# Kernel optimization log

Hardware: AMD Instinct MI355X
Metric: run time of the kernel (lower is better)

Reference implementation:

```python
import jax, jax.numpy as jnp
import numpy as np

ZONEOUT = 0.1  # eval-mode zoneout: deterministic mix prob*h_prev + (1-prob)*h_new
R = 2          # reduction_factor


def _lstm_zoneout(x, h, c, wih, whh, bih, bhh):
    g = x @ wih.T + bih + h @ whh.T + bhh
    i, f, gg, o = jnp.split(g, 4, axis=-1)
    c2 = jax.nn.sigmoid(f) * c + jax.nn.sigmoid(i) * jnp.tanh(gg)
    h2 = jax.nn.sigmoid(o) * jnp.tanh(c2)
    return ZONEOUT * h + (1 - ZONEOUT) * h2, ZONEOUT * c + (1 - ZONEOUT) * c2


def setup_inputs() -> dict:
    key = jax.random.key(0)
    ks = jax.random.split(key, 20)
    B, TENC, ENC, DEC = 64, 200, 256, 1024
    HATT, CONV, K = 128, 32, 31
    PRE, C, TFEAT = 256, 80, 1000
    s = 0.05
    def w(k, shape):
        return jax.random.normal(k, shape, jnp.float32) * s
    inp = {}
    inp['enc_output'] = jax.random.normal(ks[0], (B, TENC, ENC), jnp.float32)
    inp['text_len'] = jax.random.randint(ks[1], (B,), TENC // 2, TENC + 1, jnp.int32)
    inp['feature_target'] = jax.random.normal(ks[2], (B, C, TFEAT), jnp.float32)
    inp['att_fc_enc_w'] = w(ks[3], (HATT, ENC)); inp['att_fc_enc_b'] = jnp.zeros((HATT,), jnp.float32)
    inp['att_fc_dec_w'] = w(ks[4], (HATT, DEC))
    inp['att_fc_att_w'] = w(ks[5], (HATT, CONV))
    inp['att_loc_conv_w'] = w(ks[6], (CONV, 1, K))
    inp['att_w_w'] = w(ks[7], (1, HATT)); inp['att_w_b'] = jnp.zeros((1,), jnp.float32)
    inp['prenet_w0'] = w(ks[8], (PRE, C * R)); inp['prenet_b0'] = jnp.zeros((PRE,), jnp.float32)
    inp['prenet_w1'] = w(ks[9], (PRE, PRE)); inp['prenet_b1'] = jnp.zeros((PRE,), jnp.float32)
    inp['lstm0_wih'] = w(ks[10], (4 * DEC, ENC + PRE)); inp['lstm0_whh'] = w(ks[11], (4 * DEC, DEC))
    inp['lstm0_bih'] = jnp.zeros((4 * DEC,), jnp.float32); inp['lstm0_bhh'] = jnp.zeros((4 * DEC,), jnp.float32)
    inp['lstm1_wih'] = w(ks[12], (4 * DEC, DEC)); inp['lstm1_whh'] = w(ks[13], (4 * DEC, DEC))
    inp['lstm1_bih'] = jnp.zeros((4 * DEC,), jnp.float32); inp['lstm1_bhh'] = jnp.zeros((4 * DEC,), jnp.float32)
    inp['feat_out_w'] = w(ks[14], (C * R, ENC + DEC))
    inp['prob_out_w'] = w(ks[15], (R, ENC + DEC)); inp['prob_out_b'] = jnp.zeros((R,), jnp.float32)
    return inp


def reference(enc_output, text_len, feature_target,
              att_fc_enc_w, att_fc_enc_b, att_fc_dec_w, att_fc_att_w, att_loc_conv_w, att_w_w, att_w_b,
              prenet_w0, prenet_b0, prenet_w1, prenet_b1,
              lstm0_wih, lstm0_whh, lstm0_bih, lstm0_bhh,
              lstm1_wih, lstm1_whh, lstm1_bih, lstm1_bhh,
              feat_out_w, prob_out_w, prob_out_b):
    B, TENC, ENC = enc_output.shape
    C, T = feature_target.shape[1], feature_target.shape[2]
    S = T // R  # decoder steps (teacher forcing)
    ft = feature_target.transpose(0, 2, 1).reshape(B, S, C * R)
    pad = (att_loc_conv_w.shape[-1] - 1) // 2
    pm = enc_output @ att_fc_enc_w.T + att_fc_enc_b  # processed memory (B,T,H)
    mask = jnp.arange(TENC)[None, :] >= text_len[:, None]  # pad mask (B,T)
    DEC = lstm0_whh.shape[1]

    def attend(h0, att_prev):
        conv = jax.lax.conv_general_dilated(att_prev[:, None, :], att_loc_conv_w, (1,), [(pad, pad)],
                                            dimension_numbers=('NCH', 'OIH', 'NCH'))  # (B,conv,T)
        conv = jnp.einsum('bct,hc->bth', conv, att_fc_att_w)
        e = jnp.tanh(conv + pm + (h0 @ att_fc_dec_w.T)[:, None, :]) @ att_w_w.T + att_w_b  # (B,T,1)
        e = jnp.where(mask, -jnp.inf, e[..., 0])
        aw = jax.nn.softmax(e, axis=1)
        ac = jnp.einsum('bt,btc->bc', aw, enc_output)
        return ac, aw

    def one_step(h0, c0, h1, c1, att_prev, prev_out):
        ac, aw = attend(h0, att_prev)
        p = jax.nn.relu(prev_out @ prenet_w0.T + prenet_b0)
        p = jax.nn.relu(p @ prenet_w1.T + prenet_b1)
        xs = jnp.concatenate([ac, p], axis=1)
        h0, c0 = _lstm_zoneout(xs, h0, c0, lstm0_wih, lstm0_whh, lstm0_bih, lstm0_bhh)
        h1, c1 = _lstm_zoneout(h0, h1, c1, lstm1_wih, lstm1_whh, lstm1_bih, lstm1_bhh)
        hcs = jnp.concatenate([h1, ac], axis=1)
        return h0, c0, h1, c1, aw, hcs @ feat_out_w.T, hcs @ prob_out_w.T + prob_out_b

    z = jnp.zeros((B, DEC), enc_output.dtype)
    go = jnp.zeros((B, C * R), enc_output.dtype)
    tl = text_len[:, None].astype(enc_output.dtype)
    uniform = (~mask).astype(enc_output.dtype) / tl  # initial prev_att_w

    # step 0: uniform attention prior, go-frame input; afterwards acc = att_w (not uniform+att_w)
    h0, c0, h1, c1, aw0, out0, log0 = one_step(z, z, z, z, uniform, go)

    def scan_step(carry, prev_out):
        h0, c0, h1, c1, acc = carry
        h0, c0, h1, c1, aw, out, logit = one_step(h0, c0, h1, c1, acc, prev_out)
        return (h0, c0, h1, c1, acc + aw), (out, logit, aw)

    _, (outs, logits, aws) = jax.lax.scan(scan_step, (h0, c0, h1, c1, aw0), ft[:, :S - 1, :].transpose(1, 0, 2))
    outs = jnp.concatenate([out0[None], outs], axis=0)    # (S,B,C*R)
    logits = jnp.concatenate([log0[None], logits], axis=0)  # (S,B,R)
    aws = jnp.concatenate([aw0[None], aws], axis=0)       # (S,B,T)
    output = outs.transpose(1, 0, 2).reshape(B, S * R, C).transpose(0, 2, 1)  # (B,C,S*R)
    logit = logits.transpose(1, 0, 2).reshape(B, S * R)
    att_w = aws.transpose(1, 0, 2)  # (B,S,T)
    return output, logit, att_w
```

## Files before the change

kernel.cpp:

```cpp
#include <hip/hip_runtime.h>

#define SS 500
#define NBLKS 256
#define NSLOT 64
#define DYN_LDS 141824
#define RING 32

typedef __bf16 bf16_t;
typedef bf16_t bf16x8 __attribute__((ext_vector_type(8)));
typedef float floatx4 __attribute__((ext_vector_type(4)));

union ABu { uint4 u4; bf16x8 v; unsigned short us[8]; };

#define MFMA(a,b,c) __builtin_amdgcn_mfma_f32_16x16x32_bf16((a),(b),(c),0,0,0)

__device__ __forceinline__ float b2f(unsigned short u){
  union { unsigned int ui; float f; } x; x.ui = ((unsigned int)u) << 16; return x.f;
}
__device__ __forceinline__ unsigned short f2b(float f){
  union { float f; unsigned int ui; } x; x.f = f;
  unsigned int r = x.ui + 0x7FFFu + ((x.ui >> 16) & 1u);
  return (unsigned short)(r >> 16);
}
__device__ __forceinline__ float sigf(float x){ return 1.f/(1.f + __expf(-x)); }
__device__ __forceinline__ float tanhf_fast(float x){
  x = fminf(fmaxf(x, -15.f), 15.f);
  float e = __expf(2.f*x);
  return (e - 1.f)/(e + 1.f);
}

__device__ __forceinline__ void st_sc(unsigned short* p, unsigned short v){
  unsigned int w32 = v;
  asm volatile("global_store_short %0, %1, off sc0 sc1" :: "v"(p), "v"(w32) : "memory");
}

__device__ __forceinline__ void gbar(unsigned int* slots, unsigned int* flag,
                                     unsigned int ep, int is_master){
  asm volatile("s_waitcnt vmcnt(0)" ::: "memory");
  __syncthreads();
  if (threadIdx.x == 0){
    __hip_atomic_fetch_add(&slots[(blockIdx.x & (NSLOT-1)) * 32], 1u,
                           __ATOMIC_RELAXED, __HIP_MEMORY_SCOPE_AGENT);
  }
  if (is_master){
    if (threadIdx.x < 64){
      for(;;){
        unsigned int v = __hip_atomic_load(&slots[threadIdx.x * 32],
                                           __ATOMIC_RELAXED, __HIP_MEMORY_SCOPE_AGENT);
        int t = (int)v;
        t += __shfl_xor(t, 1);  t += __shfl_xor(t, 2);  t += __shfl_xor(t, 4);
        t += __shfl_xor(t, 8);  t += __shfl_xor(t, 16); t += __shfl_xor(t, 32);
        if ((unsigned int)t >= ep * NBLKS) break;
        __builtin_amdgcn_s_sleep(1);
      }
      __hip_atomic_store(&flag[threadIdx.x * 32], ep,
                         __ATOMIC_RELAXED, __HIP_MEMORY_SCOPE_AGENT);
    }
  } else {
    if (threadIdx.x == 0){
      unsigned int* myf = &flag[(blockIdx.x & (NSLOT-1)) * 32];
      while (__hip_atomic_load(myf, __ATOMIC_RELAXED, __HIP_MEMORY_SCOPE_AGENT) < ep)
        __builtin_amdgcn_s_sleep(2);
    }
  }
  __syncthreads();
  asm volatile("" ::: "memory");
}


__global__ void k_pm(const float* __restrict__ enc, const float* __restrict__ ew,
                     const float* __restrict__ eb, unsigned short* __restrict__ pmT){
  int id = blockIdx.x*256 + threadIdx.x;
  if (id >= 64*200*128) return;
  int h = id & 127; int bt = id >> 7;
  const float* er = enc + (size_t)bt*256;
  const float* wr = ew + (size_t)h*256;
  float a0=eb[h], a1=0.f, a2=0.f, a3=0.f;
  for (int k=0;k<256;k+=4){
    a0 += er[k]*wr[k]; a1 += er[k+1]*wr[k+1]; a2 += er[k+2]*wr[k+2]; a3 += er[k+3]*wr[k+3];
  }
  int b = bt / 200, t = bt - b*200;
  pmT[(size_t)b*25600 + (size_t)h*200 + t] = f2b((a0+a1)+(a2+a3));
}

__global__ void k_encT(const float* __restrict__ enc, unsigned short* __restrict__ encT){
  int id = blockIdx.x*256 + threadIdx.x;
  if (id >= 64*256*200) return;
  int t = id % 200; int c = (id / 200) & 255; int b = id / 51200;
  encT[id] = f2b(enc[((size_t)b*200 + t)*256 + c]);
}

__global__ void k_w2f(const float* __restrict__ attw, const float* __restrict__ convw,
                      unsigned short* __restrict__ w2f){
  __shared__ float s_w2[128*31];
  int tid = threadIdx.x;
  for (int i = tid; i < 128*31; i += 256){
    int h = i / 31, k = i % 31;
    float v = 0.f;
    for (int c=0;c<32;++c) v += attw[h*32+c]*convw[c*31+k];
    s_w2[i] = v;
  }
  __syncthreads();
  for (int i = tid; i < 512; i += 256){
    int nt = i >> 6, lane = i & 63;
    int h = nt*16 + (lane&15);
    for (int j=0;j<8;++j){
      int k = (lane>>4)*8 + j;
      w2f[(nt*64+lane)*8+j] = f2b(k < 31 ? s_w2[h*31+k] : 0.f);
    }
  }
}

__global__ void k_packlstm(const float* __restrict__ wih, const float* __restrict__ whh,
                           unsigned short* __restrict__ dst, int Kih, int NKS){
  int id = blockIdx.x*256 + threadIdx.x;
  if (id >= 128*NKS*64) return;
  int lane = id & 63; int t = id >> 6; int cu = t / NKS;
  for (int nt=0; nt<2; ++nt){
    int n = nt*16 + (lane&15);
    int du = n>>2, g = n&3;
    int row = g*1024 + cu*8 + du;
    for (int j=0;j<8;++j){
      int k = (t % NKS)*32 + ((lane>>4)*8) + j;
      float v = (k < Kih) ? wih[(size_t)row*Kih + k] : whh[(size_t)row*1024 + (k - Kih)];
      dst[((size_t)(t*2+nt)*64 + lane)*8 + j] = f2b(v);
    }
  }
}

__global__ void k_bias(const float* bi0,const float* bh0,const float* bi1,const float* bh1,
                       float* b0p, float* b1p){
  int id = blockIdx.x*256 + threadIdx.x;
  if (id >= 4096) return;
  int cu = id>>5, n = id&31, du = n>>2, g = n&3;
  int row = g*1024 + cu*8 + du;
  b0p[id] = bi0[row] + bh0[row];
  b1p[id] = bi1[row] + bh1[row];
}

__global__ void k_packgen(const float* __restrict__ src, unsigned short* __restrict__ dst,
                          int N, int K){
  int tot = (N/16)*(K/32)*64;
  int id = blockIdx.x*256 + threadIdx.x;
  if (id >= tot) return;
  int lane = id & 63; int t = id >> 6;
  int nks = K/32;
  int n = (t / nks)*16 + (lane&15);
  for (int j=0;j<8;++j){
    int k = (t % nks)*32 + (lane>>4)*8 + j;
    dst[((size_t)t*64 + lane)*8 + j] = f2b(src[(size_t)n*K + k]);
  }
}

__global__ void k_woutp(const float* __restrict__ fw, const float* __restrict__ pw,
                        unsigned short* __restrict__ dst){
  int id = blockIdx.x*256 + threadIdx.x;
  if (id >= 11*40*64) return;
  int lane = id & 63; int t = id >> 6;
  int n = (t/40)*16 + (lane&15);
  for (int j=0;j<8;++j){
    int k = (t%40)*32 + (lane>>4)*8 + j;
    float v = 0.f;
    if (n < 160) v = fw[(size_t)n*1280 + k];
    else if (n < 162) v = pw[(size_t)(n-160)*1280 + k];
    dst[((size_t)t*64 + lane)*8 + j] = f2b(v);
  }
}

__global__ void k_pre1(const float* __restrict__ ftgt, const unsigned short* __restrict__ w0p,
                       const float* __restrict__ b0, unsigned short* __restrict__ C1){
  int mt = blockIdx.x;
  int tid = threadIdx.x, w = tid>>6, L = tid&63, ccol = L&15, q = L>>4;
  int sb0 = mt*16; int s = sb0 >> 6; int b0r = sb0 & 63;
  floatx4 z = {0.f,0.f,0.f,0.f};
  floatx4 acc[4] = {z,z,z,z};
  for (int ks=0; ks<5; ++ks){
    ABu av;
    if (s == 0){ av.u4.x=0; av.u4.y=0; av.u4.z=0; av.u4.w=0; }
    else {
      int b = b0r + ccol;
      for (int j=0;j<8;++j){
        int jj = ks*32 + q*8 + j;
        av.us[j] = f2b(ftgt[(size_t)b*80000 + (size_t)(jj%80)*1000 + (size_t)(s-1)*2 + (jj/80)]);
      }
    }
    for (int i=0;i<4;++i){
      ABu bf; bf.u4 = *(const uint4*)(w0p + ((size_t)((w*4+i)*5 + ks)*64 + L)*8);
      acc[i] = MFMA(av.v, bf.v, acc[i]);
    }
  }
  for (int i=0;i<4;++i){
    int icol = (w*4+i)*16 + ccol;
    float bia = b0[icol];
    for (int r=0;r<4;++r){
      int sb = sb0 + q*4 + r;
      C1[(size_t)sb*256 + icol] = f2b(fmaxf(acc[i][r] + bia, 0.f));
    }
  }
}

__global__ void k_pre2(const unsigned short* __restrict__ C1, const unsigned short* __restrict__ w1p,
                       const float* __restrict__ b1, unsigned short* __restrict__ P){
  int mt = blockIdx.x;
  int tid = threadIdx.x, w = tid>>6, L = tid&63, ccol = L&15, q = L>>4;
  int sb0 = mt*16;
  floatx4 z = {0.f,0.f,0.f,0.f};
  floatx4 acc[4] = {z,z,z,z};
  for (int ks=0; ks<8; ++ks){
    ABu av; av.u4 = *(const uint4*)(C1 + (size_t)(sb0+ccol)*256 + ks*32 + q*8);
    for (int i=0;i<4;++i){
      ABu bf; bf.u4 = *(const uint4*)(w1p + ((size_t)((w*4+i)*8 + ks)*64 + L)*8);
      acc[i] = MFMA(av.v, bf.v, acc[i]);
    }
  }
  for (int i=0;i<4;++i){
    int icol = (w*4+i)*16 + ccol;
    float bia = b1[icol];
    for (int r=0;r<4;++r){
      int sb = sb0 + q*4 + r;
      P[(size_t)sb*256 + icol] = f2b(fmaxf(acc[i][r] + bia, 0.f));
    }
  }
}


struct PArgs {
  const int* tlen;
  const float* ww; const float* wwb; const float* probb;
  const unsigned short* pmT; const unsigned short* encT;
  const unsigned short* W2f; const unsigned short* Wdecf;
  const unsigned short* W0p; const unsigned short* W1p;
  const float* b0p; const float* b1p;
  const unsigned short* P; const unsigned short* Woutp;
  unsigned short* xh0; unsigned short* xh1; unsigned short* acbf;
  unsigned int* bar; unsigned int* flag;
  float* dout;
};

__global__ __launch_bounds__(256, 1) void k_decoder(PArgs A)
{
  const int cu = blockIdx.x;
  const int tid = threadIdx.x;
  const int w = tid>>6, L = tid&63;
  const int ccol = L&15, q = L>>4;
  const int is_master = (cu == NBLKS-1);

  extern __shared__ char pool[];
  unsigned short* sW = (unsigned short*)pool;
  float* sGB; float* sCST; float* sBIAS;
  if (cu < 128){
    sGB   = (float*)(pool + 98304);
    sCST  = (float*)(pool + 106752);
    sBIAS = (float*)(pool + 108800);
  } else {
    sGB   = (float*)(pool + 131072);
    sCST  = (float*)(pool + 139520);
    sBIAS = (float*)(pool + 141568);
  }

  __shared__ unsigned short s_ahi[240], s_alo[240];
  __shared__ unsigned short s_h0[1024];
  __shared__ float s_e[256];
  __shared__ float s_red[16];
  __shared__ float s_dp[128];
  __shared__ float s_ww[128];

  if (cu < 128){
    const unsigned short* src = A.W0p + (size_t)cu*48*2*512;
    for (int i = tid*8; i < 48*2*512; i += 2048)
      *(uint4*)(sW + i) = *(const uint4*)(src + i);
    if (tid < 32) sBIAS[tid] = A.b0p[cu*32 + tid];
  } else {
    const unsigned short* src = A.W1p + (size_t)(cu-128)*64*2*512;
    for (int i = tid*8; i < 64*2*512; i += 2048)
      *(uint4*)(sW + i) = *(const uint4*)(src + i);
    if (tid < 32) sBIAS[tid] = A.b1p[(cu-128)*32 + tid];
  }
  for (int i = tid; i < 512; i += 256) sCST[i] = 0.f;

  float accv = 0.f; int lenb = 0; float wwbv = 0.f;
  ABu w2fr[8];
  if (cu < 64) {
    lenb = A.tlen[cu];
    wwbv = A.wwb[0];
    float inv = 1.f / (float)lenb;
    for (int i = tid; i < 240; i += 256) {
      int t = i - 15;
      float v = (t >= 0 && t < 200 && t < lenb) ? inv : 0.f;
      unsigned short hi = f2b(v);
      s_ahi[i] = hi; s_alo[i] = f2b(v - b2f(hi));
    }
    if (tid < 200) accv = (tid < lenb) ? inv : 0.f;
    if (tid < 128) s_ww[tid] = A.ww[tid];
    #pragma unroll
    for (int nt=0; nt<8; ++nt) w2fr[nt].u4 = *(const uint4*)(A.W2f + (nt*64 + L)*8);
  }

  unsigned int ep = 0;
  gbar(A.bar, A.flag, ++ep, is_master);
  __builtin_amdgcn_fence(__ATOMIC_ACQUIRE, "agent");

  for (int s = 0; s <= SS+1; ++s) {
    if (cu < 64 && s < SS) {
      const int b = cu;
      const unsigned short* xh0r = A.xh0 + (size_t)((s+RING-1)&(RING-1))*65536;
      if (tid < 128) *(uint4*)(s_h0 + tid*8) = *(const uint4*)(xh0r + b*1024 + tid*8);
      __syncthreads();
      {
        uint4 p0[8], p1[8];
        #pragma unroll
        for (int k=0;k<8;++k){
          p0[k] = *(const uint4*)(A.Wdecf + (size_t)((w*2+0)*32+k)*512 + (size_t)L*8);
          p1[k] = *(const uint4*)(A.Wdecf + (size_t)((w*2+1)*32+k)*512 + (size_t)L*8);
        }
        floatx4 acc0 = {0.f,0.f,0.f,0.f}, acc1 = {0.f,0.f,0.f,0.f};
        #pragma unroll
        for (int ks=0; ks<32; ++ks){
          ABu bf0, bf1; bf0.u4 = p0[ks&7]; bf1.u4 = p1[ks&7];
          if (ks+8 < 32){
            p0[ks&7] = *(const uint4*)(A.Wdecf + (size_t)((w*2+0)*32+ks+8)*512 + (size_t)L*8);
            p1[ks&7] = *(const uint4*)(A.Wdecf + (size_t)((w*2+1)*32+ks+8)*512 + (size_t)L*8);
          }
          ABu av;
          if (ccol == 0) av.u4 = *(const uint4*)(s_h0 + ks*32 + q*8);
          else { av.u4.x=0; av.u4.y=0; av.u4.z=0; av.u4.w=0; }
          acc0 = MFMA(av.v, bf0.v, acc0);
          acc1 = MFMA(av.v, bf1.v, acc1);
        }
        if (L < 16){
          s_dp[(w*2+0)*16 + ccol] = acc0[0];
          s_dp[(w*2+1)*16 + ccol] = acc1[0];
        }
      }
      __syncthreads();
      {
        const unsigned short* pmrowT = A.pmT + (size_t)b*25600;
        for (int mt = w; mt < 13; mt += 4) {
          ABu ahi, alo;
          int abase = mt*16 + ccol + q*8;
          for (int j=0;j<8;++j){ ahi.us[j] = s_ahi[abase+j]; alo.us[j] = s_alo[abase+j]; }
          floatx4 acc[8];
          for (int nt=0;nt<8;++nt){
            floatx4 zz = {0.f,0.f,0.f,0.f};
            zz = MFMA(ahi.v, w2fr[nt].v, zz);
            zz = MFMA(alo.v, w2fr[nt].v, zz);
            acc[nt] = zz;
          }
          int t0 = mt*16 + q*4;
          union { ushort4 v; unsigned short us[4]; } pv[8];
          #pragma unroll
          for (int nt=0;nt<8;++nt)
            pv[nt].v = *(const ushort4*)(pmrowT + (size_t)(nt*16+ccol)*200 + t0);
          #pragma unroll
          for (int r=0;r<4;++r){
            int t = t0 + r;
            float part = 0.f;
            if (t < 200) {
              #pragma unroll
              for (int nt=0;nt<8;++nt){
                int h = nt*16 + ccol;
                float v = acc[nt][r] + b2f(pv[nt].us[r]) + s_dp[h];
                part += s_ww[h] * tanhf_fast(v);
              }
            }
            part += __shfl_xor(part, 1);
            part += __shfl_xor(part, 2);
            part += __shfl_xor(part, 4);
            part += __shfl_xor(part, 8);
            if (t < 200 && ccol == 0)
              s_e[t] = (t < lenb) ? (part + wwbv) : -1e30f;
          }
        }
      }
      __syncthreads();
      {
        float v = (tid < 200) ? s_e[tid] : -1e30f;
        float m = v;
        for (int o=1;o<64;o<<=1) m = fmaxf(m, __shfl_xor(m, o));
        if (L == 0) s_red[w] = m;
        __syncthreads();
        m = fmaxf(fmaxf(s_red[0], s_red[1]), fmaxf(s_red[2], s_red[3]));
        float ex = (tid < 200) ? __expf(v - m) : 0.f;
        float sm = ex;
        for (int o=1;o<64;o<<=1) sm += __shfl_xor(sm, o);
        if (L == 0) s_red[8+w] = sm;
        __syncthreads();
        float inv = 1.f / (s_red[8]+s_red[9]+s_red[10]+s_red[11]);
        if (tid < 200){
          float aw = ex * inv;
          s_e[tid] = aw;
          A.dout[5184000 + (size_t)b*100000 + (size_t)s*200 + tid] = aw;
          accv = (s == 0) ? aw : (accv + aw);
          unsigned short hi = f2b(accv);
          s_ahi[15+tid] = hi; s_alo[15+tid] = f2b(accv - b2f(hi));
        }
      }
      __syncthreads();
      {
        const unsigned short* er = A.encT + (size_t)b*51200 + (size_t)tid*200;
        float a0=0.f,a1=0.f,a2=0.f,a3=0.f;
        #pragma unroll 5
        for (int it=0; it<25; ++it){
          ABu v; v.u4 = *(const uint4*)(er + it*8);
          a0 += s_e[it*8+0]*b2f(v.us[0]); a1 += s_e[it*8+1]*b2f(v.us[1]);
          a2 += s_e[it*8+2]*b2f(v.us[2]); a3 += s_e[it*8+3]*b2f(v.us[3]);
          a0 += s_e[it*8+4]*b2f(v.us[4]); a1 += s_e[it*8+5]*b2f(v.us[5]);
          a2 += s_e[it*8+6]*b2f(v.us[6]); a3 += s_e[it*8+7]*b2f(v.us[7]);
        }
        st_sc(A.acbf + (size_t)(s&(RING-1))*16384 + b*256 + tid, f2b((a0+a1)+(a2+a3)));
      }
    }
    if (cu >= 75 && cu < 119 && s >= 2) {
      const int nt = (cu-75) % 11; const int mg = (cu-75) / 11;
      const int s2 = s - 2;
      const unsigned short* segH  = A.xh1 + (size_t)(s2&(RING-1))*65536;
      const unsigned short* segAC = A.acbf + (size_t)(s2&(RING-1))*16384;
      const unsigned short* wo = A.Woutp + (size_t)nt*40*512;
      const int brow = mg*16 + ccol;
      uint4 ap[10], wp[10];
      #pragma unroll
      for (int kk=0; kk<10; ++kk){
        int ks = w*10 + kk;
        ap[kk] = *(const uint4*)((ks < 32) ? (segH + (size_t)brow*1024 + ks*32 + q*8)
                                           : (segAC + (size_t)brow*256 + (ks-32)*32 + q*8));
        wp[kk] = *(const uint4*)(wo + (size_t)ks*512 + (size_t)L*8);
      }
      floatx4 acc = {0.f,0.f,0.f,0.f};
      #pragma unroll
      for (int kk=0; kk<10; ++kk){
        ABu av, bf; av.u4 = ap[kk]; bf.u4 = wp[kk];
        acc = MFMA(av.v, bf.v, acc);
      }
      #pragma unroll
      for (int r=0;r<4;++r) sGB[w*256 + (q*4+r)*16 + ccol] = acc[r];
      __syncthreads();
      {
        float v = sGB[tid] + sGB[256+tid] + sGB[512+tid] + sGB[768+tid];
        int blocal = tid>>4, colp = tid&15;
        int j = nt*16 + colp; int bb = mg*16 + blocal;
        if (j < 160){
          int rr = j/80, cc2 = j%80;
          A.dout[(size_t)bb*80000 + (size_t)cc2*1000 + s2*2 + rr] = v;
        } else if (j < 162){
          A.dout[5120000 + (size_t)bb*1000 + s2*2 + (j-160)] = v + A.probb[j-160];
        }
      }
      __syncthreads();
    }
    if (cu >= 128 && s >= 1 && s <= SS) {
      const int cp = cu - 128;
      const unsigned short* segA = A.xh0 + (size_t)((s+RING-1)&(RING-1))*65536;
      const unsigned short* segB = A.xh1 + (size_t)((s+RING-2)&(RING-1))*65536;
      const int brow = w*16 + ccol;
      uint4 pp[16];
      #pragma unroll
      for (int t=0;t<16;++t)
        pp[t] = *(const uint4*)(segA + (size_t)brow*1024 + t*32 + q*8);
      floatx4 a0 = {0.f,0.f,0.f,0.f}, a1 = {0.f,0.f,0.f,0.f};
      #pragma unroll
      for (int t=0;t<64;++t){
        ABu av; av.u4 = pp[t&15];
        ABu b0f, b1f;
        b0f.u4 = *(const uint4*)(sW + (size_t)(t*2+0)*512 + L*8);
        b1f.u4 = *(const uint4*)(sW + (size_t)(t*2+1)*512 + L*8);
        if (t+16 < 64){
          int t2 = t+16;
          const unsigned short* sp = (t2 < 32) ? (segA + (size_t)brow*1024 + t2*32 + q*8)
                                               : (segB + (size_t)brow*1024 + (t2-32)*32 + q*8);
          pp[t&15] = *(const uint4*)sp;
        }
        a0 = MFMA(av.v, b0f.v, a0);
        a1 = MFMA(av.v, b1f.v, a1);
      }
      #pragma unroll
      for (int r=0;r<4;++r){
        int bb = w*16 + q*4 + r;
        sGB[bb*33 + ccol]      = a0[r] + sBIAS[ccol];
        sGB[bb*33 + 16 + ccol] = a1[r] + sBIAS[16+ccol];
      }
      __syncthreads();
      unsigned short* xout = A.xh1 + (size_t)((s+RING-1)&(RING-1))*65536;
      const unsigned short* hprev = segB;
      for (int rep=0;rep<2;++rep){
        int cell = tid + rep*256;
        int du = cell>>6, bb = cell&63;
        float gi=sGB[bb*33+du*4+0], gf=sGB[bb*33+du*4+1];
        float gg=sGB[bb*33+du*4+2], go=sGB[bb*33+du*4+3];
        float cprev = sCST[du*64+bb];
        float c2 = sigf(gf)*cprev + sigf(gi)*tanhf_fast(gg);
        float h2 = sigf(go)*tanhf_fast(c2);
        float cn = 0.1f*cprev + 0.9f*c2;
        float hp = b2f(hprev[(size_t)bb*1024 + cp*8 + du]);
        float hn = 0.1f*hp + 0.9f*h2;
        sCST[du*64+bb] = cn;
        st_sc(xout + (size_t)bb*1024 + cp*8 + du, f2b(hn));
      }
    }
    uint4 pre[16];
    const unsigned short *l0P = nullptr, *l0H = nullptr, *l0AC = nullptr;
    if (cu < 128 && s < SS){
      l0AC = A.acbf + (size_t)(s&(RING-1))*16384;
      l0P  = A.P + (size_t)s*16384;
      l0H  = A.xh0 + (size_t)((s+RING-1)&(RING-1))*65536;
      const int brow = w*16 + ccol;
      #pragma unroll
      for (int t=0;t<8;++t)
        pre[t]   = *(const uint4*)(l0P + (size_t)brow*256 + t*32 + q*8);
      #pragma unroll
      for (int t=0;t<8;++t)
        pre[8+t] = *(const uint4*)(l0H + (size_t)brow*1024 + t*32 + q*8);
    }
    gbar(A.bar, A.flag, ++ep, is_master);
    if (cu < 128 && s < SS) {
      const int brow = w*16 + ccol;
      floatx4 a0 = {0.f,0.f,0.f,0.f}, a1 = {0.f,0.f,0.f,0.f};
      #pragma unroll
      for (int t=0;t<48;++t){
        ABu av; av.u4 = pre[t&15];
        int ow = (t < 8) ? (8+t) : ((t < 40) ? (16+(t-8)) : (t-40));
        ABu b0f, b1f;
        b0f.u4 = *(const uint4*)(sW + (size_t)(ow*2+0)*512 + L*8);
        b1f.u4 = *(const uint4*)(sW + (size_t)(ow*2+1)*512 + L*8);
        if (t+16 < 48){
          int t2 = t+16;
          const unsigned short* sp = (t2 < 40) ? (l0H + (size_t)brow*1024 + (t2-8)*32 + q*8)
                                               : (l0AC + (size_t)brow*256 + (t2-40)*32 + q*8);
          pre[t&15] = *(const uint4*)sp;
        }
        a0 = MFMA(av.v, b0f.v, a0);
        a1 = MFMA(av.v, b1f.v, a1);
      }
      #pragma unroll
      for (int r=0;r<4;++r){
        int bb = w*16 + q*4 + r;
        sGB[bb*33 + ccol]      = a0[r] + sBIAS[ccol];
        sGB[bb*33 + 16 + ccol] = a1[r] + sBIAS[16+ccol];
      }
      __syncthreads();
      unsigned short* xout = A.xh0 + (size_t)(s&(RING-1))*65536;
      const unsigned short* hprev = l0H;
      for (int rep=0;rep<2;++rep){
        int cell = tid + rep*256;
        int du = cell>>6, bb = cell&63;
        float gi=sGB[bb*33+du*4+0], gf=sGB[bb*33+du*4+1];
        float gg=sGB[bb*33+du*4+2], go=sGB[bb*33+du*4+3];
        float cprev = sCST[du*64+bb];
        float c2 = sigf(gf)*cprev + sigf(gi)*tanhf_fast(gg);
        float h2 = sigf(go)*tanhf_fast(c2);
        float cn = 0.1f*cprev + 0.9f*c2;
        float hp = b2f(hprev[(size_t)bb*1024 + cu*8 + du]);
        float hn = 0.1f*hp + 0.9f*h2;
        sCST[du*64+bb] = cn;
        st_sc(xout + (size_t)bb*1024 + cu*8 + du, f2b(hn));
      }
    }
    gbar(A.bar, A.flag, ++ep, is_master);
    if ((s & 15) == 8) __builtin_amdgcn_fence(__ATOMIC_ACQUIRE, "agent");
  }
}


extern "C" void kernel_launch(void* const* d_in, const int* in_sizes, int n_in,
                              void* d_out, int out_size, void* d_ws, size_t ws_size,
                              hipStream_t stream)
{
  const float* enc   = (const float*)d_in[0];
  const int*   tlen  = (const int*)d_in[1];
  const float* ftgt  = (const float*)d_in[2];
  const float* aew   = (const float*)d_in[3];
  const float* aeb   = (const float*)d_in[4];
  const float* adw   = (const float*)d_in[5];
  const float* aaw   = (const float*)d_in[6];
  const float* acw   = (const float*)d_in[7];
  const float* aww   = (const float*)d_in[8];
  const float* awb   = (const float*)d_in[9];
  const float* pw0   = (const float*)d_in[10];
  const float* pb0   = (const float*)d_in[11];
  const float* pw1   = (const float*)d_in[12];
  const float* pb1   = (const float*)d_in[13];
  const float* l0wih = (const float*)d_in[14];
  const float* l0whh = (const float*)d_in[15];
  const float* l0bih = (const float*)d_in[16];
  const float* l0bhh = (const float*)d_in[17];
  const float* l1wih = (const float*)d_in[18];
  const float* l1whh = (const float*)d_in[19];
  const float* l1bih = (const float*)d_in[20];
  const float* l1bhh = (const float*)d_in[21];
  const float* fow   = (const float*)d_in[22];
  const float* pow_  = (const float*)d_in[23];
  const float* pob   = (const float*)d_in[24];
  float* dout = (float*)d_out;

  char* ws = (char*)d_ws;
  size_t off = 0;
  auto alloc = [&](size_t bytes)->void*{
    void* p = (void*)(ws + off);
    off += (bytes + 255) & ~(size_t)255;
    return p;
  };

  unsigned short* pmT   = (unsigned short*)alloc((size_t)64*200*128*2 + 256);
  unsigned short* encT  = (unsigned short*)alloc((size_t)64*256*200*2);
  unsigned short* W2f   = (unsigned short*)alloc((size_t)8*64*8*2);
  unsigned short* Wdecf = (unsigned short*)alloc((size_t)8*32*64*8*2);
  unsigned short* W0p   = (unsigned short*)alloc((size_t)128*48*2*512*2);
  unsigned short* W1p   = (unsigned short*)alloc((size_t)128*64*2*512*2);
  float* b0p            = (float*)alloc((size_t)4096*4);
  float* b1p            = (float*)alloc((size_t)4096*4);
  unsigned short* w0pp  = (unsigned short*)alloc((size_t)16*5*512*2);
  unsigned short* w1pp  = (unsigned short*)alloc((size_t)16*8*512*2);
  unsigned short* C1    = (unsigned short*)alloc((size_t)32000*256*2);
  unsigned short* P     = (unsigned short*)alloc((size_t)32000*256*2);
  unsigned short* Woutp = (unsigned short*)alloc((size_t)11*40*512*2);
  unsigned short* xh0   = (unsigned short*)alloc((size_t)RING*65536*2);
  unsigned short* xh1   = (unsigned short*)alloc((size_t)RING*65536*2);
  unsigned short* acbf  = (unsigned short*)alloc((size_t)RING*16384*2);
  unsigned int* bar     = (unsigned int*)alloc((size_t)NSLOT*128);
  unsigned int* flag    = (unsigned int*)alloc((size_t)NSLOT*128);

  hipMemsetAsync(bar, 0, (size_t)NSLOT*128, stream);
  hipMemsetAsync(flag, 0, (size_t)NSLOT*128, stream);
  hipMemsetAsync(xh0, 0, (size_t)RING*65536*2, stream);
  hipMemsetAsync(xh1, 0, (size_t)RING*65536*2, stream);
  hipMemsetAsync(acbf, 0, (size_t)RING*16384*2, stream);

  k_pm     <<<6400, 256, 0, stream>>>(enc, aew, aeb, pmT);
  k_encT   <<<12800,256, 0, stream>>>(enc, encT);
  k_w2f    <<<1,    256, 0, stream>>>(aaw, acw, W2f);
  k_packgen<<<64,   256, 0, stream>>>(adw, Wdecf, 128, 1024);
  k_packlstm<<<1536,256, 0, stream>>>(l0wih, l0whh, W0p, 512, 48);
  k_packlstm<<<2048,256, 0, stream>>>(l1wih, l1whh, W1p, 1024, 64);
  k_bias   <<<16,   256, 0, stream>>>(l0bih, l0bhh, l1bih, l1bhh, b0p, b1p);
  k_packgen<<<20,   256, 0, stream>>>(pw0, w0pp, 256, 160);
  k_packgen<<<32,   256, 0, stream>>>(pw1, w1pp, 256, 256);
  k_woutp  <<<110,  256, 0, stream>>>(fow, pow_, Woutp);
  k_pre1   <<<2000, 256, 0, stream>>>(ftgt, w0pp, pb0, C1);
  k_pre2   <<<2000, 256, 0, stream>>>(C1, w1pp, pb1, P);

  PArgs A;
  A.tlen = tlen; A.ww = aww; A.wwb = awb; A.probb = pob;
  A.pmT = pmT; A.encT = encT; A.W2f = W2f; A.Wdecf = Wdecf;
  A.W0p = W0p; A.W1p = W1p; A.b0p = b0p; A.b1p = b1p;
  A.P = P; A.Woutp = Woutp;
  A.xh0 = xh0; A.xh1 = xh1; A.acbf = acbf;
  A.bar = bar; A.flag = flag; A.dout = dout;

  hipFuncSetAttribute((const void*)k_decoder,
                      hipFuncAttributeMaxDynamicSharedMemorySize, DYN_LDS);
  k_decoder<<<NBLKS, 256, DYN_LDS, stream>>>(A);
}
```

Measured before the change: 16.91 ms.

## Pipeline decoder stages across dedicated block roles with one barrier per tick

Reassigns the persistent decoder's blocks to dedicated roles: attention, a separate decoder-projection stage, output projection, and LSTM layers 0 and 1. Stages run skewed by one tick each, so every step needs a single global barrier instead of two. The projection moves from the attention blocks into its own blocks that stage weights in LDS and pass results through a ring buffer. Each LSTM block now covers twice as many gate columns, streaming half its weights from global memory with prefetch while the other half sits in LDS. This adds pipeline latency and more global traffic per LSTM block, and it idles 12 blocks.

After: 14.53 ms. 1.16x faster.

```diff
diff --git a/kernel.cpp b/kernel.cpp
--- a/kernel.cpp
+++ b/kernel.cpp
@@ -3,7 +3,7 @@
 #define SS 500
 #define NBLKS 256
 #define NSLOT 64
-#define DYN_LDS 141824
+#define DYN_LDS 152064
 #define RING 32
 
 typedef __bf16 bf16_t;
@@ -11,6 +11,7 @@
 typedef float floatx4 __attribute__((ext_vector_type(4)));
 
 union ABu { uint4 u4; bf16x8 v; unsigned short us[8]; };
+union USu { ushort4 v; unsigned short us[4]; };
 
 #define MFMA(a,b,c) __builtin_amdgcn_mfma_f32_16x16x32_bf16((a),(b),(c),0,0,0)
 
@@ -32,6 +33,9 @@
 __device__ __forceinline__ void st_sc(unsigned short* p, unsigned short v){
   unsigned int w32 = v;
   asm volatile("global_store_short %0, %1, off sc0 sc1" :: "v"(p), "v"(w32) : "memory");
+}
+__device__ __forceinline__ void st_scf(float* p, float v){
+  asm volatile("global_store_dword %0, %1, off sc0 sc1" :: "v"(p), "v"(v) : "memory");
 }
 
 __device__ __forceinline__ void gbar(unsigned int* slots, unsigned int* flag,
@@ -233,6 +237,7 @@
   const float* b0p; const float* b1p;
   const unsigned short* P; const unsigned short* Woutp;
   unsigned short* xh0; unsigned short* xh1; unsigned short* acbf;
+  float* dpbuf;
   unsigned int* bar; unsigned int* flag;
   float* dout;
 };
@@ -245,42 +250,59 @@
   const int ccol = L&15, q = L>>4;
   const int is_master = (cu == NBLKS-1);
 
+  const int R_ATT = (cu < 64);
+  const int R_DP  = (cu >= 64 && cu < 72);
+  const int R_OUT = (cu >= 72 && cu < 116);
+  const int R_L0  = (cu >= 116 && cu < 180);
+  const int R_L1  = (cu >= 180 && cu < 244);
+
   extern __shared__ char pool[];
-  unsigned short* sW = (unsigned short*)pool;
-  float* sGB; float* sCST; float* sBIAS;
-  if (cu < 128){
-    sGB   = (float*)(pool + 98304);
-    sCST  = (float*)(pool + 106752);
-    sBIAS = (float*)(pool + 108800);
-  } else {
-    sGB   = (float*)(pool + 131072);
-    sCST  = (float*)(pool + 139520);
-    sBIAS = (float*)(pool + 141568);
-  }
+  unsigned short* sW   = (unsigned short*)pool;
+  float* sGB = nullptr; float* sCST = nullptr; float* sBIAS = nullptr; float* sRED = nullptr;
+  if (R_L0){ sGB = (float*)(pool + 98304);  sCST = (float*)(pool + 114944); sBIAS = (float*)(pool + 119040); }
+  if (R_L1){ sGB = (float*)(pool + 131072); sCST = (float*)(pool + 147712); sBIAS = (float*)(pool + 151808); }
+  if (R_OUT){ sRED = (float*)(pool + 40960); }
 
   __shared__ unsigned short s_ahi[240], s_alo[240];
-  __shared__ unsigned short s_h0[1024];
   __shared__ float s_e[256];
   __shared__ float s_red[16];
-  __shared__ float s_dp[128];
   __shared__ float s_ww[128];
 
-  if (cu < 128){
-    const unsigned short* src = A.W0p + (size_t)cu*48*2*512;
-    for (int i = tid*8; i < 48*2*512; i += 2048)
+  const int g0 = cu - 116;
+  const int g1 = cu - 180;
+  const int dpid = cu - 64;
+  const int dmg = dpid >> 1, dng = dpid & 1;
+  const int oid = cu - 72;
+  const int ont = oid % 11, omg = oid / 11;
+
+  if (R_L0){
+    const unsigned short* src = A.W0p + (size_t)(2*g0)*49152;
+    for (int i = tid*8; i < 49152; i += 2048)
       *(uint4*)(sW + i) = *(const uint4*)(src + i);
-    if (tid < 32) sBIAS[tid] = A.b0p[cu*32 + tid];
-  } else {
-    const unsigned short* src = A.W1p + (size_t)(cu-128)*64*2*512;
-    for (int i = tid*8; i < 64*2*512; i += 2048)
+    if (tid < 64) sBIAS[tid] = A.b0p[g0*64 + tid];
+    for (int i = tid; i < 1024; i += 256) sCST[i] = 0.f;
+  }
+  if (R_L1){
+    const unsigned short* src = A.W1p + (size_t)(2*g1)*65536;
+    for (int i = tid*8; i < 65536; i += 2048)
       *(uint4*)(sW + i) = *(const uint4*)(src + i);
-    if (tid < 32) sBIAS[tid] = A.b1p[(cu-128)*32 + tid];
-  }
-  for (int i = tid; i < 512; i += 256) sCST[i] = 0.f;
+    if (tid < 64) sBIAS[tid] = A.b1p[g1*64 + tid];
+    for (int i = tid; i < 1024; i += 256) sCST[i] = 0.f;
+  }
+  if (R_DP){
+    const unsigned short* src = A.Wdecf + (size_t)dng*4*32*512;
+    for (int i = tid*8; i < 65536; i += 2048)
+      *(uint4*)(sW + i) = *(const uint4*)(src + i);
+  }
+  if (R_OUT){
+    const unsigned short* src = A.Woutp + (size_t)ont*40*512;
+    for (int i = tid*8; i < 40*512; i += 2048)
+      *(uint4*)(sW + i) = *(const uint4*)(src + i);
+  }
 
   float accv = 0.f; int lenb = 0; float wwbv = 0.f;
   ABu w2fr[8];
-  if (cu < 64) {
+  if (R_ATT) {
     lenb = A.tlen[cu];
     wwbv = A.wwb[0];
     float inv = 1.f / (float)lenb;
@@ -300,76 +322,100 @@
   gbar(A.bar, A.flag, ++ep, is_master);
   __builtin_amdgcn_fence(__ATOMIC_ACQUIRE, "agent");
 
-  for (int s = 0; s <= SS+1; ++s) {
-    if (cu < 64 && s < SS) {
+  for (int tick = 0; tick <= SS+3; ++tick) {
+    const int s_att = tick - 1;
+    const int s_l0  = tick - 2;
+    const int s_l1  = tick - 3;
+    const int s_p   = tick - 4;
+
+    uint4 pA[8], pW2[8], pW3[8];
+    const unsigned short *l0AC = nullptr, *l0P = nullptr, *l0H = nullptr;
+    const unsigned short *l1A = nullptr, *l1B = nullptr;
+    const unsigned short *Wst = nullptr;
+    const int l0_act = R_L0 && (s_l0 >= 0 && s_l0 < SS);
+    const int l1_act = R_L1 && (s_l1 >= 0 && s_l1 < SS);
+    if (l0_act){
+      l0AC = A.acbf + (size_t)(s_l0&(RING-1))*16384;
+      l0P  = A.P + (size_t)s_l0*16384;
+      l0H  = A.xh0 + (size_t)((s_l0+RING-1)&(RING-1))*65536;
+      Wst  = A.W0p + (size_t)(2*g0+1)*49152;
+      const int brow = w*16 + ccol;
+      #pragma unroll
+      for (int t=0;t<8;++t){
+        pA[t]  = *(const uint4*)(l0P + (size_t)brow*256 + t*32 + q*8);
+        int ow = 8+t;
+        pW2[t] = *(const uint4*)(Wst + (size_t)(ow*2+0)*512 + L*8);
+        pW3[t] = *(const uint4*)(Wst + (size_t)(ow*2+1)*512 + L*8);
+      }
+    }
+    if (l1_act){
+      l1A = A.xh0 + (size_t)(s_l1&(RING-1))*65536;
+      l1B = A.xh1 + (size_t)((s_l1+RING-1)&(RING-1))*65536;
+      Wst = A.W1p + (size_t)(2*g1+1)*65536;
+      #pragma unroll
+      for (int t=0;t<8;++t){
+        pW2[t] = *(const uint4*)(Wst + (size_t)(t*2+0)*512 + L*8);
+        pW3[t] = *(const uint4*)(Wst + (size_t)(t*2+1)*512 + L*8);
+      }
+    }
+
+    gbar(A.bar, A.flag, ++ep, is_master);
+
+    if (R_ATT && s_att >= 0 && s_att < SS) {
       const int b = cu;
-      const unsigned short* xh0r = A.xh0 + (size_t)((s+RING-1)&(RING-1))*65536;
-      if (tid < 128) *(uint4*)(s_h0 + tid*8) = *(const uint4*)(xh0r + b*1024 + tid*8);
-      __syncthreads();
+      const int slot = s_att & (RING-1);
+      float dpv[8];
       {
-        uint4 p0[8], p1[8];
+        const float* dpp = A.dpbuf + (size_t)slot*8192 + b*128 + ccol;
         #pragma unroll
-        for (int k=0;k<8;++k){
-          p0[k] = *(const uint4*)(A.Wdecf + (size_t)((w*2+0)*32+k)*512 + (size_t)L*8);
-          p1[k] = *(const uint4*)(A.Wdecf + (size_t)((w*2+1)*32+k)*512 + (size_t)L*8);
-        }
-        floatx4 acc0 = {0.f,0.f,0.f,0.f}, acc1 = {0.f,0.f,0.f,0.f};
-        #pragma unroll
-        for (int ks=0; ks<32; ++ks){
-          ABu bf0, bf1; bf0.u4 = p0[ks&7]; bf1.u4 = p1[ks&7];
-          if (ks+8 < 32){
-            p0[ks&7] = *(const uint4*)(A.Wdecf + (size_t)((w*2+0)*32+ks+8)*512 + (size_t)L*8);
-            p1[ks&7] = *(const uint4*)(A.Wdecf + (size_t)((w*2+1)*32+ks+8)*512 + (size_t)L*8);
-          }
-          ABu av;
-          if (ccol == 0) av.u4 = *(const uint4*)(s_h0 + ks*32 + q*8);
-          else { av.u4.x=0; av.u4.y=0; av.u4.z=0; av.u4.w=0; }
-          acc0 = MFMA(av.v, bf0.v, acc0);
-          acc1 = MFMA(av.v, bf1.v, acc1);
-        }
-        if (L < 16){
-          s_dp[(w*2+0)*16 + ccol] = acc0[0];
-          s_dp[(w*2+1)*16 + ccol] = acc1[0];
-        }
-      }
-      __syncthreads();
-      {
-        const unsigned short* pmrowT = A.pmT + (size_t)b*25600;
-        for (int mt = w; mt < 13; mt += 4) {
-          ABu ahi, alo;
-          int abase = mt*16 + ccol + q*8;
-          for (int j=0;j<8;++j){ ahi.us[j] = s_ahi[abase+j]; alo.us[j] = s_alo[abase+j]; }
-          floatx4 acc[8];
-          for (int nt=0;nt<8;++nt){
-            floatx4 zz = {0.f,0.f,0.f,0.f};
-            zz = MFMA(ahi.v, w2fr[nt].v, zz);
-            zz = MFMA(alo.v, w2fr[nt].v, zz);
-            acc[nt] = zz;
-          }
+        for (int nt=0;nt<8;++nt) dpv[nt] = dpp[nt*16];
+      }
+      USu pv[4][8];
+      #pragma unroll
+      for (int i=0;i<4;++i){
+        int mt = w + i*4;
+        if (mt < 13){
           int t0 = mt*16 + q*4;
-          union { ushort4 v; unsigned short us[4]; } pv[8];
           #pragma unroll
           for (int nt=0;nt<8;++nt)
-            pv[nt].v = *(const ushort4*)(pmrowT + (size_t)(nt*16+ccol)*200 + t0);
-          #pragma unroll
-          for (int r=0;r<4;++r){
-            int t = t0 + r;
-            float part = 0.f;
-            if (t < 200) {
-              #pragma unroll
-              for (int nt=0;nt<8;++nt){
-                int h = nt*16 + ccol;
-                float v = acc[nt][r] + b2f(pv[nt].us[r]) + s_dp[h];
-                part += s_ww[h] * tanhf_fast(v);
-              }
+            pv[i][nt].v = *(const ushort4*)(A.pmT + (size_t)b*25600 + (size_t)(nt*16+ccol)*200 + t0);
+        }
+      }
+      #pragma unroll
+      for (int i=0;i<4;++i){
+        int mt = w + i*4;
+        if (mt >= 13) continue;
+        ABu ahi, alo;
+        int abase = mt*16 + ccol + q*8;
+        #pragma unroll
+        for (int j=0;j<8;++j){ ahi.us[j] = s_ahi[abase+j]; alo.us[j] = s_alo[abase+j]; }
+        floatx4 acc[8];
+        #pragma unroll
+        for (int nt=0;nt<8;++nt){
+          floatx4 zz = {0.f,0.f,0.f,0.f};
+          zz = MFMA(ahi.v, w2fr[nt].v, zz);
+          zz = MFMA(alo.v, w2fr[nt].v, zz);
+          acc[nt] = zz;
+        }
+        int t0 = mt*16 + q*4;
+        #pragma unroll
+        for (int r=0;r<4;++r){
+          int t = t0 + r;
+          float part = 0.f;
+          if (t < 200) {
+            #pragma unroll
+            for (int nt=0;nt<8;++nt){
+              int h = nt*16 + ccol;
+              float v = acc[nt][r] + b2f(pv[i][nt].us[r]) + dpv[nt];
+              part += s_ww[h] * tanhf_fast(v);
             }
-            part += __shfl_xor(part, 1);
-            part += __shfl_xor(part, 2);
-            part += __shfl_xor(part, 4);
-            part += __shfl_xor(part, 8);
-            if (t < 200 && ccol == 0)
-              s_e[t] = (t < lenb) ? (part + wwbv) : -1e30f;
           }
+          part += __shfl_xor(part, 1);
+          part += __shfl_xor(part, 2);
+          part += __shfl_xor(part, 4);
+          part += __shfl_xor(part, 8);
+          if (t < 200 && ccol == 0)
+            s_e[t] = (t < lenb) ? (part + wwbv) : -1e30f;
         }
       }
       __syncthreads();
@@ -389,8 +435,8 @@
         if (tid < 200){
           float aw = ex * inv;
           s_e[tid] = aw;
-          A.dout[5184000 + (size_t)b*100000 + (size_t)s*200 + tid] = aw;
-          accv = (s == 0) ? aw : (accv + aw);
+          A.dout[5184000 + (size_t)b*100000 + (size_t)s_att*200 + tid] = aw;
+          accv = (s_att == 0) ? aw : (accv + aw);
           unsigned short hi = f2b(accv);
           s_ahi[15+tid] = hi; s_alo[15+tid] = f2b(accv - b2f(hi));
         }
@@ -407,155 +453,175 @@
           a0 += s_e[it*8+4]*b2f(v.us[4]); a1 += s_e[it*8+5]*b2f(v.us[5]);
           a2 += s_e[it*8+6]*b2f(v.us[6]); a3 += s_e[it*8+7]*b2f(v.us[7]);
         }
-        st_sc(A.acbf + (size_t)(s&(RING-1))*16384 + b*256 + tid, f2b((a0+a1)+(a2+a3)));
-      }
-    }
-    if (cu >= 75 && cu < 119 && s >= 2) {
-      const int nt = (cu-75) % 11; const int mg = (cu-75) / 11;
-      const int s2 = s - 2;
-      const unsigned short* segH  = A.xh1 + (size_t)(s2&(RING-1))*65536;
-      const unsigned short* segAC = A.acbf + (size_t)(s2&(RING-1))*16384;
-      const unsigned short* wo = A.Woutp + (size_t)nt*40*512;
-      const int brow = mg*16 + ccol;
-      uint4 ap[10], wp[10];
+        st_sc(A.acbf + (size_t)slot*16384 + b*256 + tid, f2b((a0+a1)+(a2+a3)));
+      }
+    }
+
+    if (R_DP && tick < SS) {
+      const unsigned short* h0r = A.xh0 + (size_t)((tick+RING-1)&(RING-1))*65536;
+      const int brow = dmg*16 + ccol;
+      uint4 pd[16];
+      #pragma unroll
+      for (int t=0;t<16;++t) pd[t] = *(const uint4*)(h0r + (size_t)brow*1024 + t*32 + q*8);
+      floatx4 acc = {0.f,0.f,0.f,0.f};
+      #pragma unroll
+      for (int ks=0; ks<32; ++ks){
+        ABu av; av.u4 = pd[ks&15];
+        ABu bf; bf.u4 = *(const uint4*)(sW + (size_t)(w*32+ks)*512 + L*8);
+        if (ks+16 < 32) pd[ks&15] = *(const uint4*)(h0r + (size_t)brow*1024 + (ks+16)*32 + q*8);
+        acc = MFMA(av.v, bf.v, acc);
+      }
+      float* dpo = A.dpbuf + (size_t)(tick&(RING-1))*8192;
+      #pragma unroll
+      for (int r=0;r<4;++r){
+        int b = dmg*16 + q*4 + r;
+        int col = dng*64 + w*16 + ccol;
+        st_scf(dpo + (size_t)b*128 + col, acc[r]);
+      }
+    }
+
+    if (R_OUT && s_p >= 0 && s_p < SS) {
+      const unsigned short* segH  = A.xh1 + (size_t)(s_p&(RING-1))*65536;
+      const unsigned short* segAC = A.acbf + (size_t)(s_p&(RING-1))*16384;
+      const int brow = omg*16 + ccol;
+      uint4 ap[10];
       #pragma unroll
       for (int kk=0; kk<10; ++kk){
         int ks = w*10 + kk;
         ap[kk] = *(const uint4*)((ks < 32) ? (segH + (size_t)brow*1024 + ks*32 + q*8)
                                            : (segAC + (size_t)brow*256 + (ks-32)*32 + q*8));
-        wp[kk] = *(const uint4*)(wo + (size_t)ks*512 + (size_t)L*8);
       }
       floatx4 acc = {0.f,0.f,0.f,0.f};
       #pragma unroll
       for (int kk=0; kk<10; ++kk){
-        ABu av, bf; av.u4 = ap[kk]; bf.u4 = wp[kk];
+        ABu av, bf; av.u4 = ap[kk];
+        bf.u4 = *(const uint4*)(sW + (size_t)(w*10+kk)*512 + L*8);
         acc = MFMA(av.v, bf.v, acc);
       }
       #pragma unroll
-      for (int r=0;r<4;++r) sGB[w*256 + (q*4+r)*16 + ccol] = acc[r];
+      for (int r=0;r<4;++r) sRED[w*256 + (q*4+r)*16 + ccol] = acc[r];
       __syncthreads();
       {
-        float v = sGB[tid] + sGB[256+tid] + sGB[512+tid] + sGB[768+tid];
+        float v = sRED[tid] + sRED[256+tid] + sRED[512+tid] + sRED[768+tid];
         int blocal = tid>>4, colp = tid&15;
-        int j = nt*16 + colp; int bb = mg*16 + blocal;
+        int j = ont*16 + colp; int bb = omg*16 + blocal;
         if (j < 160){
           int rr = j/80, cc2 = j%80;
-          A.dout[(size_t)bb*80000 + (size_t)cc2*1000 + s2*2 + rr] = v;
+          A.dout[(size_t)bb*80000 + (size_t)cc2*1000 + s_p*2 + rr] = v;
         } else if (j < 162){
-          A.dout[5120000 + (size_t)bb*1000 + s2*2 + (j-160)] = v + A.probb[j-160];
+          A.dout[5120000 + (size_t)bb*1000 + s_p*2 + (j-160)] = v + A.probb[j-160];
         }
       }
-      __syncthreads();
-    }
-    if (cu >= 128 && s >= 1 && s <= SS) {
-      const int cp = cu - 128;
-      const unsigned short* segA = A.xh0 + (size_t)((s+RING-1)&(RING-1))*65536;
-      const unsigned short* segB = A.xh1 + (size_t)((s+RING-2)&(RING-1))*65536;
+    }
+
+    if (l0_act) {
       const int brow = w*16 + ccol;
-      uint4 pp[16];
-      #pragma unroll
-      for (int t=0;t<16;++t)
-        pp[t] = *(const uint4*)(segA + (size_t)brow*1024 + t*32 + q*8);
-      floatx4 a0 = {0.f,0.f,0.f,0.f}, a1 = {0.f,0.f,0.f,0.f};
-      #pragma unroll
-      for (int t=0;t<64;++t){
-        ABu av; av.u4 = pp[t&15];
-        ABu b0f, b1f;
-        b0f.u4 = *(const uint4*)(sW + (size_t)(t*2+0)*512 + L*8);
-        b1f.u4 = *(const uint4*)(sW + (size_t)(t*2+1)*512 + L*8);
-        if (t+16 < 64){
-          int t2 = t+16;
-          const unsigned short* sp = (t2 < 32) ? (segA + (size_t)brow*1024 + t2*32 + q*8)
-                                               : (segB + (size_t)brow*1024 + (t2-32)*32 + q*8);
-          pp[t&15] = *(const uint4*)sp;
+      floatx4 a0 = {0.f,0.f,0.f,0.f}, a1 = a0, a2 = a0, a3 = a0;
+      #pragma unroll
+      for (int t=0;t<48;++t){
+        ABu av; av.u4 = pA[t&7];
+        int ow = (t < 40) ? (t+8) : (t-40);
+        ABu b0f, b1f, b2f_, b3f;
+        b0f.u4 = *(const uint4*)(sW + (size_t)(ow*2+0)*512 + L*8);
+        b1f.u4 = *(const uint4*)(sW + (size_t)(ow*2+1)*512 + L*8);
+        b2f_.u4 = pW2[t&7]; b3f.u4 = pW3[t&7];
+        if (t+8 < 48){
+          int t2 = t+8;
+          const unsigned short* sp = (t2 < 40) ? (l0H + (size_t)brow*1024 + (t2-8)*32 + q*8)
+                                               : (l0AC + (size_t)brow*256 + (t2-40)*32 + q*8);
+          pA[t&7] = *(const uint4*)sp;
+          int ow2 = (t2 < 40) ? (t2+8) : (t2-40);
+          pW2[t&7] = *(const uint4*)(Wst + (size_t)(ow2*2+0)*512 + L*8);
+          pW3[t&7] = *(const uint4*)(Wst + (size_t)(ow2*2+1)*512 + L*8);
         }
         a0 = MFMA(av.v, b0f.v, a0);
         a1 = MFMA(av.v, b1f.v, a1);
+        a2 = MFMA(av.v, b2f_.v, a2);
+        a3 = MFMA(av.v, b3f.v, a3);
       }
       #pragma unroll
       for (int r=0;r<4;++r){
         int bb = w*16 + q*4 + r;
-        sGB[bb*33 + ccol]      = a0[r] + sBIAS[ccol];
-        sGB[bb*33 + 16 + ccol] = a1[r] + sBIAS[16+ccol];
+        sGB[bb*65 +      ccol] = a0[r] + sBIAS[ccol];
+        sGB[bb*65 + 16 + ccol] = a1[r] + sBIAS[16+ccol];
+        sGB[bb*65 + 32 + ccol] = a2[r] + sBIAS[32+ccol];
+        sGB[bb*65 + 48 + ccol] = a3[r] + sBIAS[48+ccol];
       }
       __syncthreads();
-      unsigned short* xout = A.xh1 + (size_t)((s+RING-1)&(RING-1))*65536;
-      const unsigned short* hprev = segB;
-      for (int rep=0;rep<2;++rep){
+      unsigned short* xout = A.xh0 + (size_t)(s_l0&(RING-1))*65536;
+      #pragma unroll
+      for (int rep=0;rep<4;++rep){
         int cell = tid + rep*256;
         int du = cell>>6, bb = cell&63;
-        float gi=sGB[bb*33+du*4+0], gf=sGB[bb*33+du*4+1];
-        float gg=sGB[bb*33+du*4+2], go=sGB[bb*33+du*4+3];
+        int cb = (du>>3)*32 + (du&7)*4;
+        float gi=sGB[bb*65+cb+0], gf=sGB[bb*65+cb+1];
+        float gg=sGB[bb*65+cb+2], go=sGB[bb*65+cb+3];
         float cprev = sCST[du*64+bb];
         float c2 = sigf(gf)*cprev + sigf(gi)*tanhf_fast(gg);
         float h2 = sigf(go)*tanhf_fast(c2);
         float cn = 0.1f*cprev + 0.9f*c2;
-        float hp = b2f(hprev[(size_t)bb*1024 + cp*8 + du]);
+        float hp = b2f(l0H[(size_t)bb*1024 + g0*16 + du]);
         float hn = 0.1f*hp + 0.9f*h2;
         sCST[du*64+bb] = cn;
-        st_sc(xout + (size_t)bb*1024 + cp*8 + du, f2b(hn));
-      }
-    }
-    uint4 pre[16];
-    const unsigned short *l0P = nullptr, *l0H = nullptr, *l0AC = nullptr;
-    if (cu < 128 && s < SS){
-      l0AC = A.acbf + (size_t)(s&(RING-1))*16384;
-      l0P  = A.P + (size_t)s*16384;
-      l0H  = A.xh0 + (size_t)((s+RING-1)&(RING-1))*65536;
+        st_sc(xout + (size_t)bb*1024 + g0*16 + du, f2b(hn));
+      }
+    }
+
+    if (l1_act) {
       const int brow = w*16 + ccol;
       #pragma unroll
       for (int t=0;t<8;++t)
-        pre[t]   = *(const uint4*)(l0P + (size_t)brow*256 + t*32 + q*8);
-      #pragma unroll
-      for (int t=0;t<8;++t)
-        pre[8+t] = *(const uint4*)(l0H + (size_t)brow*1024 + t*32 + q*8);
-    }
-    gbar(A.bar, A.flag, ++ep, is_master);
-    if (cu < 128 && s < SS) {
-      const int brow = w*16 + ccol;
-      floatx4 a0 = {0.f,0.f,0.f,0.f}, a1 = {0.f,0.f,0.f,0.f};
-      #pragma unroll
-      for (int t=0;t<48;++t){
-        ABu av; av.u4 = pre[t&15];
-        int ow = (t < 8) ? (8+t) : ((t < 40) ? (16+(t-8)) : (t-40));
-        ABu b0f, b1f;
-        b0f.u4 = *(const uint4*)(sW + (size_t)(ow*2+0)*512 + L*8);
-        b1f.u4 = *(const uint4*)(sW + (size_t)(ow*2+1)*512 + L*8);
-        if (t+16 < 48){
-          int t2 = t+16;
-          const unsigned short* sp = (t2 < 40) ? (l0H + (size_t)brow*1024 + (t2-8)*32 + q*8)
-                                               : (l0AC + (size_t)brow*256 + (t2-40)*32 + q*8);
-          pre[t&15] = *(const uint4*)sp;
+        pA[t] = *(const uint4*)(l1A + (size_t)brow*1024 + t*32 + q*8);
+      floatx4 a0 = {0.f,0.f,0.f,0.f}, a1 = a0, a2 = a0, a3 = a0;
+      #pragma unroll
+      for (int t=0;t<64;++t){
+        ABu av; av.u4 = pA[t&7];
+        ABu b0f, b1f, b2f_, b3f;
+        b0f.u4 = *(const uint4*)(sW + (size_t)(t*2+0)*512 + L*8);
+        b1f.u4 = *(const uint4*)(sW + (size_t)(t*2+1)*512 + L*8);
+        b2f_.u4 = pW2[t&7]; b3f.u4 = pW3[t&7];
+        if (t+8 < 64){
+          int t2 = t+8;
+          const unsigned short* sp = (t2 < 32) ? (l1A + (size_t)brow*1024 + t2*32 + q*8)
+                                               : (l1B + (size_t)brow*1024 + (t2-32)*32 + q*8);
+          pA[t&7] = *(const uint4*)sp;
+          pW2[t&7] = *(const uint4*)(Wst + (size_t)(t2*2+0)*512 + L*8);
+          pW3[t&7] = *(const uint4*)(Wst + (size_t)(t2*2+1)*512 + L*8);
         }
         a0 = MFMA(av.v, b0f.v, a0);
         a1 = MFMA(av.v, b1f.v, a1);
+        a2 = MFMA(av.v, b2f_.v, a2);
+        a3 = MFMA(av.v, b3f.v, a3);
       }
       #pragma unroll
       for (int r=0;r<4;++r){
         int bb = w*16 + q*4 + r;
-        sGB[bb*33 + ccol]      = a0[r] + sBIAS[ccol];
-        sGB[bb*33 + 16 + ccol] = a1[r] + sBIAS[16+ccol];
+        sGB[bb*65 +      ccol] = a0[r] + sBIAS[ccol];
+        sGB[bb*65 + 16 + ccol] = a1[r] + sBIAS[16+ccol];
+        sGB[bb*65 + 32 + ccol] = a2[r] + sBIAS[32+ccol];
+        sGB[bb*65 + 48 + ccol] = a3[r] + sBIAS[48+ccol];
       }
       __syncthreads();
-      unsigned short* xout = A.xh0 + (size_t)(s&(RING-1))*65536;
-      const unsigned short* hprev = l0H;
-      for (int rep=0;rep<2;++rep){
+      unsigned short* xout = A.xh1 + (size_t)(s_l1&(RING-1))*65536;
+      #pragma unroll
+      for (int rep=0;rep<4;++rep){
         int cell = tid + rep*256;
         int du = cell>>6, bb = cell&63;
-        float gi=sGB[bb*33+du*4+0], gf=sGB[bb*33+du*4+1];
-        float gg=sGB[bb*33+du*4+2], go=sGB[bb*33+du*4+3];
+        int cb = (du>>3)*32 + (du&7)*4;
+        float gi=sGB[bb*65+cb+0], gf=sGB[bb*65+cb+1];
+        float gg=sGB[bb*65+cb+2], go=sGB[bb*65+cb+3];
         float cprev = sCST[du*64+bb];
         float c2 = sigf(gf)*cprev + sigf(gi)*tanhf_fast(gg);
         float h2 = sigf(go)*tanhf_fast(c2);
         float cn = 0.1f*cprev + 0.9f*c2;
-        float hp = b2f(hprev[(size_t)bb*1024 + cu*8 + du]);
+        float hp = b2f(l1B[(size_t)bb*1024 + g1*16 + du]);
         float hn = 0.1f*hp + 0.9f*h2;
         sCST[du*64+bb] = cn;
-        st_sc(xout + (size_t)bb*1024 + cu*8 + du, f2b(hn));
-      }
-    }
-    gbar(A.bar, A.flag, ++ep, is_master);
-    if ((s & 15) == 8) __builtin_amdgcn_fence(__ATOMIC_ACQUIRE, "agent");
+        st_sc(xout + (size_t)bb*1024 + g1*16 + du, f2b(hn));
+      }
+    }
+
+    if ((tick & 15) == 8) __builtin_amdgcn_fence(__ATOMIC_ACQUIRE, "agent");
   }
 }
 
@@ -615,6 +681,7 @@
   unsigned short* xh0   = (unsigned short*)alloc((size_t)RING*65536*2);
   unsigned short* xh1   = (unsigned short*)alloc((size_t)RING*65536*2);
   unsigned short* acbf  = (unsigned short*)alloc((size_t)RING*16384*2);
+  float* dpbuf          = (float*)alloc((size_t)RING*8192*4);
   unsigned int* bar     = (unsigned int*)alloc((size_t)NSLOT*128);
   unsigned int* flag    = (unsigned int*)alloc((size_t)NSLOT*128);
 
@@ -642,7 +709,7 @@
   A.pmT = pmT; A.encT = encT; A.W2f = W2f; A.Wdecf = Wdecf;
   A.W0p = W0p; A.W1p = W1p; A.b0p = b0p; A.b1p = b1p;
   A.P = P; A.Woutp = Woutp;
-  A.xh0 = xh0; A.xh1 = xh1; A.acbf = acbf;
+  A.xh0 = xh0; A.xh1 = xh1; A.acbf = acbf; A.dpbuf = dpbuf;
   A.bar = bar; A.flag = flag; A.dout = dout;
 
   hipFuncSetAttribute((const void*)k_decoder,
```
